# Optimization experiments

Hardware: AMD Instinct MI355X
Metric: run time of the kernel (lower is better)

The kernel has to match this reference:

```python
import jax, jax.numpy as jnp
import numpy as np

N = 50000       # total nodes
D = 20000       # disease nodes (first D rows)
M = 30000       # mirna nodes
E = 800000      # edges
DSIM = 512; MSIM = 512
HID = 128; OUT = 128; P = 3   # powers p = [0,1,2]
PAIRS = 100000


def _lin(k, o, i):
    s = 1.0 / np.sqrt(i)
    return jax.random.uniform(k, (o, i), jnp.float32, -s, s)


def setup_inputs() -> dict:
    key = jax.random.key(0)
    ks = jax.random.split(key, 24)
    inp = {}
    inp["d_sim"] = jax.random.normal(ks[0], (N, DSIM), jnp.float32)
    inp["m_sim"] = jax.random.normal(ks[1], (N, MSIM), jnp.float32)
    inp["edge_src"] = jax.random.randint(ks[2], (E,), 0, N, jnp.int32)
    inp["edge_dst"] = jax.random.randint(ks[3], (E,), 0, N, jnp.int32)
    inp["src"] = jax.random.randint(ks[4], (PAIRS,), 0, D, jnp.int32)
    inp["dst"] = D + jax.random.randint(ks[5], (PAIRS,), 0, M, jnp.int32)
    # input projections
    inp["d_fc_w"] = _lin(ks[6], HID, DSIM); inp["d_fc_b"] = jnp.zeros((HID,), jnp.float32)
    inp["m_fc_w"] = _lin(ks[7], HID, MSIM); inp["m_fc_b"] = jnp.zeros((HID,), jnp.float32)
    # MixHopConv per-power weights (no bias)
    inp["l0_w"] = jnp.stack([_lin(ks[8 + j], OUT, HID) for j in range(P)])         # [P, OUT, HID]
    inp["l1_w"] = jnp.stack([_lin(ks[11 + j], HID, OUT * P) for j in range(P)])    # [P, HID, OUT*P]
    inp["fc_w"] = _lin(ks[14], OUT, HID * P)
    inp["d_fc1_w"] = _lin(ks[15], OUT, OUT + DSIM); inp["d_fc1_b"] = jnp.zeros((OUT,), jnp.float32)
    inp["m_fc1_w"] = _lin(ks[16], OUT, OUT + MSIM); inp["m_fc1_b"] = jnp.zeros((OUT,), jnp.float32)
    # predictor MLP
    inp["p0_w"] = _lin(ks[17], OUT, 2 * OUT); inp["p0_b"] = jnp.zeros((OUT,), jnp.float32)
    inp["p1_w"] = _lin(ks[18], 1, OUT); inp["p1_b"] = jnp.zeros((1,), jnp.float32)
    return inp


def _mixhop(feats, Ws, edge_src, edge_dst, norm):
    """DGL MixHopConv with p=[0,1,2]: outputs [W_j (D^-1/2 A D^-1/2)^j X for j in p], concatenated."""
    outs = []
    for j in range(P):
        outs.append(feats @ Ws[j].T)
        if j < P - 1:  # propagate one more hop (last hop's propagation is unused)
            feats = feats * norm
            feats = jax.ops.segment_sum(feats[edge_src], edge_dst, num_segments=N)
            feats = feats * norm
    return jnp.concatenate(outs, axis=1)


def reference(d_sim, m_sim, edge_src, edge_dst, src, dst,
              d_fc_w, d_fc_b, m_fc_w, m_fc_b, l0_w, l1_w, fc_w,
              d_fc1_w, d_fc1_b, m_fc1_w, m_fc1_b, p0_w, p0_b, p1_w, p1_b):
    # symmetric normalization from in-degrees (clamped to >= 1)
    degs = jax.ops.segment_sum(jnp.ones((E,), jnp.float32), edge_dst, num_segments=N)
    norm = (jnp.maximum(degs, 1.0) ** -0.5)[:, None]  # [N, 1]
    # per-node-type input projection (dropout = identity in eval)
    z_d = d_sim[:D] @ d_fc_w.T + d_fc_b
    z_m = m_sim[D:] @ m_fc_w.T + m_fc_b
    feats = jnp.concatenate([z_d, z_m], axis=0)               # [N, HID]
    feats = _mixhop(feats, l0_w, edge_src, edge_dst, norm)    # [N, OUT*P]
    feats = _mixhop(feats, l1_w, edge_src, edge_dst, norm)    # [N, HID*P]
    feats = feats @ fc_w.T                                    # [N, OUT]
    h_d = jax.nn.elu(jnp.concatenate([feats[:D], d_sim[:D]], axis=1) @ d_fc1_w.T + d_fc1_b)
    h_m = jax.nn.elu(jnp.concatenate([feats[D:], m_sim[D:]], axis=1) @ m_fc1_w.T + m_fc1_b)
    h = jnp.concatenate([h_d, h_m], axis=0)                   # [N, OUT]
    hc = jnp.concatenate([h[src], h[dst]], axis=1)            # [PAIRS, 2*OUT]
    score = jax.nn.sigmoid(jax.nn.relu(hc @ p0_w.T + p0_b) @ p1_w.T + p1_b)
    return score
```

## Files before the change

kernel.cpp:

```cpp
#include <hip/hip_runtime.h>
#include <cstddef>
#include <cstdint>

#define N_NODES 50000
#define D_NODES 20000
#define M_NODES 30000
#define E_EDGES 800000
#define PAIRS_N 100000

typedef unsigned short u16;
typedef unsigned int u32;
typedef short bf16x8 __attribute__((ext_vector_type(8)));
typedef float f32x4 __attribute__((ext_vector_type(4)));

__device__ __forceinline__ float bf2f(u16 u) {
  u32 v = ((u32)u) << 16;
  return __builtin_bit_cast(float, v);
}
__device__ __forceinline__ u16 f2bf(float f) {
  u32 u = __builtin_bit_cast(u32, f);
  u32 r = (u + 0x7fffu + ((u >> 16) & 1u)) >> 16;
  return (u16)r;
}
__device__ __forceinline__ u32 pk2(float x, float y) {
  return (u32)f2bf(x) | ((u32)f2bf(y) << 16);
}

__global__ void simconv_kernel(const float* __restrict__ dsim, const float* __restrict__ msim,
                               u16* __restrict__ out) {
  int i = blockIdx.x * 256 + threadIdx.x;
  if (i >= N_NODES * 64) return;
  int row = i >> 6, c8 = (i & 63) << 3;
  const float* p = ((row < D_NODES) ? dsim : msim) + (size_t)row * 512 + c8;
  float4 f0 = ((const float4*)p)[0];
  float4 f1 = ((const float4*)p)[1];
  *(uint4*)(out + (size_t)i * 8) =
      make_uint4(pk2(f0.x, f0.y), pk2(f0.z, f0.w), pk2(f1.x, f1.y), pk2(f1.z, f1.w));
}

__global__ void wconv_kernel(const float* s0, const float* s1, const float* s2,
                             const float* s3, const float* s4,
                             u16* d0, u16* d1, u16* d2, u16* d3, u16* d4) {
  int i = blockIdx.x * 256 + threadIdx.x;
  const float* s; u16* d; int l;
  if      (i < 16384) { s = s0; d = d0; l = i; }
  else if (i < 32768) { s = s1; d = d1; l = i - 16384; }
  else if (i < 53248) { s = s2; d = d2; l = i - 32768; }
  else if (i < 73728) { s = s3; d = d3; l = i - 53248; }
  else if (i < 81920) { s = s4; d = d4; l = i - 73728; }
  else return;
  float4 v = *(const float4*)(s + (size_t)l * 4);
  ushort4 o;
  o.x = f2bf(v.x); o.y = f2bf(v.y); o.z = f2bf(v.z); o.w = f2bf(v.w);
  *(ushort4*)(d + (size_t)l * 4) = o;
}

__global__ void wcomb1_kernel(const float* __restrict__ l1w, const float* __restrict__ l0w,
                              float* __restrict__ Tmp) {
  int pj = blockIdx.x;
  int p = pj / 3, j = pj % 3;
  int o = blockIdx.y;
  int i = threadIdx.x;
  const float* wp = l1w + (size_t)p * 49152 + (size_t)o * 384 + 128 * j;
  const float* wj = l0w + (size_t)j * 16384 + i;
  float acc = 0.f;
#pragma unroll 4
  for (int t = 0; t < 128; ++t) acc += wp[t] * wj[(size_t)t * 128];
  Tmp[(size_t)pj * 16384 + (size_t)o * 128 + i] = acc;
}
__global__ void wcomb2_kernel(const float* __restrict__ fcw, const float* __restrict__ Tmp,
                              u16* __restrict__ G) {
  int k = blockIdx.x;
  int of = blockIdx.y;
  int i = threadIdx.x;
  float acc = 0.f;
  int plo = (k > 2) ? (k - 2) : 0;
  int phi = (k < 2) ? k : 2;
  for (int p = plo; p <= phi; ++p) {
    int j = k - p;
    const float* fp = fcw + (size_t)of * 384 + 128 * p;
    const float* tp = Tmp + (size_t)(p * 3 + j) * 16384 + i;
#pragma unroll 4
    for (int t = 0; t < 128; ++t) acc += fp[t] * tp[(size_t)t * 128];
  }
  G[(size_t)of * 640 + 128 * k + i] = f2bf(acc);
}

__global__ void zero_int_kernel(int* p, int n) {
  int i = blockIdx.x * 256 + threadIdx.x;
  if (i < n) p[i] = 0;
}
__global__ void deg_count_kernel(const int* __restrict__ dst, int* __restrict__ degs, int e) {
  int i = blockIdx.x * 256 + threadIdx.x;
  if (i < e) atomicAdd(&degs[dst[i]], 1);
}
__global__ void norm_reduce_kernel(const int* __restrict__ degs, float* __restrict__ norm,
                                   int n, int* __restrict__ bsums) {
  __shared__ int s[256];
  int t = threadIdx.x;
  int i = blockIdx.x * 256 + t;
  int d = (i < n) ? degs[i] : 0;
  if (i < n) norm[i] = rsqrtf(fmaxf((float)d, 1.0f));
  s[t] = d;
  __syncthreads();
  for (int st = 128; st > 0; st >>= 1) {
    if (t < st) s[t] += s[t + st];
    __syncthreads();
  }
  if (t == 0) bsums[blockIdx.x] = s[0];
}
__global__ void scan_small_kernel(int* b, int nb) {
  __shared__ int s[256];
  int t = threadIdx.x;
  int orig = (t < nb) ? b[t] : 0;
  s[t] = orig;
  __syncthreads();
  for (int st = 1; st < 256; st <<= 1) {
    int v = (t >= st) ? s[t - st] : 0;
    __syncthreads();
    s[t] += v;
    __syncthreads();
  }
  if (t < nb) b[t] = s[t] - orig;
}
__global__ void scan_final_kernel(const int* __restrict__ degs, const int* __restrict__ boff,
                                  int* __restrict__ out, int* __restrict__ cursor,
                                  int n, int total) {
  __shared__ int s[256];
  int t = threadIdx.x;
  int i = blockIdx.x * 256 + t;
  int orig = (i < n) ? degs[i] : 0;
  s[t] = orig;
  __syncthreads();
  for (int st = 1; st < 256; st <<= 1) {
    int v = (t >= st) ? s[t - st] : 0;
    __syncthreads();
    s[t] += v;
    __syncthreads();
  }
  if (i < n) {
    int v = boff[blockIdx.x] + s[t] - orig;
    out[i] = v;
    cursor[i] = v;
  }
  if (i == 0) out[n] = total;
}
__global__ void fill_csr_kernel(const int* __restrict__ esrc, const int* __restrict__ edst,
                                int* __restrict__ cursor, int* __restrict__ csr_src, int e) {
  int i = blockIdx.x * 256 + threadIdx.x;
  if (i < e) {
    int p = atomicAdd(&cursor[edst[i]], 1);
    csr_src[p] = esrc[i];
  }
}

__global__ void prop_kernel(const u16* __restrict__ in,
                            u16* __restrict__ outu, int ldu, int cOff,
                            u16* __restrict__ outs,
                            const int* __restrict__ off, const int* __restrict__ srcs,
                            const float* __restrict__ norm, int nnodes) {
  const int node = blockIdx.x * 4 + (threadIdx.x >> 6);
  if (node >= nnodes) return;
  const int lane = threadIdx.x & 63;
  const int e0 = off[node], e1 = off[node + 1];
  float a0 = 0.f, a1 = 0.f;
  const u16* basec = in + (lane << 1);
  for (int base = e0; base < e1; base += 64) {
    int nE = e1 - base; if (nE > 64) nE = 64;
    int myE = srcs[base + ((lane < nE) ? lane : (nE - 1))];
    int i = 0;
    for (; i + 8 <= nE; i += 8) {
      int s0 = __builtin_amdgcn_readlane(myE, i + 0);
      int s1 = __builtin_amdgcn_readlane(myE, i + 1);
      int s2 = __builtin_amdgcn_readlane(myE, i + 2);
      int s3 = __builtin_amdgcn_readlane(myE, i + 3);
      int s4 = __builtin_amdgcn_readlane(myE, i + 4);
      int s5 = __builtin_amdgcn_readlane(myE, i + 5);
      int s6 = __builtin_amdgcn_readlane(myE, i + 6);
      int s7 = __builtin_amdgcn_readlane(myE, i + 7);
      u32 v0 = *(const u32*)(basec + ((size_t)s0 << 7));
      u32 v1 = *(const u32*)(basec + ((size_t)s1 << 7));
      u32 v2 = *(const u32*)(basec + ((size_t)s2 << 7));
      u32 v3 = *(const u32*)(basec + ((size_t)s3 << 7));
      u32 v4 = *(const u32*)(basec + ((size_t)s4 << 7));
      u32 v5 = *(const u32*)(basec + ((size_t)s5 << 7));
      u32 v6 = *(const u32*)(basec + ((size_t)s6 << 7));
      u32 v7 = *(const u32*)(basec + ((size_t)s7 << 7));
      a0 += bf2f((u16)v0); a1 += bf2f((u16)(v0 >> 16));
      a0 += bf2f((u16)v1); a1 += bf2f((u16)(v1 >> 16));
      a0 += bf2f((u16)v2); a1 += bf2f((u16)(v2 >> 16));
      a0 += bf2f((u16)v3); a1 += bf2f((u16)(v3 >> 16));
      a0 += bf2f((u16)v4); a1 += bf2f((u16)(v4 >> 16));
      a0 += bf2f((u16)v5); a1 += bf2f((u16)(v5 >> 16));
      a0 += bf2f((u16)v6); a1 += bf2f((u16)(v6 >> 16));
      a0 += bf2f((u16)v7); a1 += bf2f((u16)(v7 >> 16));
    }
    for (; i < nE; ++i) {
      int s = __builtin_amdgcn_readlane(myE, i);
      u32 v = *(const u32*)(basec + ((size_t)s << 7));
      a0 += bf2f((u16)v); a1 += bf2f((u16)(v >> 16));
    }
  }
  float nd = norm[node];
  *(u32*)(outu + (size_t)node * ldu + cOff + (lane << 1)) = pk2(a0 * nd, a1 * nd);
  if (outs) {
    float nd2 = nd * nd;
    *(u32*)(outs + ((size_t)node << 7) + (lane << 1)) = pk2(a0 * nd2, a1 * nd2);
  }
}

__global__ __launch_bounds__(256) void mfma_gemm_kernel(
    const u16* __restrict__ A1, int lda1, int K1,
    const u16* __restrict__ A2, int lda2, int K2,
    const int* __restrict__ gsrc, const int* __restrict__ gdst,
    const u16* __restrict__ Wa, const u16* __restrict__ Wb,
    const float* __restrict__ biasa, const float* __restrict__ biasb,
    int splitB, int rowD, int boundA, int nrows,
    u16* __restrict__ Cu, int ldcu, int colOff,
    u16* __restrict__ Cs, const float* __restrict__ normp,
    const float* __restrict__ p1w, const float* __restrict__ p1b, float* __restrict__ outf,
    int act) {
  __shared__ u32 As[32 * 32];
  __shared__ u32 Ws[128 * 32];
  const int tid = threadIdx.x;
  const bool segb = (int)blockIdx.x >= splitB;
  const int brow = segb ? rowD + ((int)blockIdx.x - splitB) * 32 : (int)blockIdx.x * 32;
  const int bound = segb ? nrows : boundA;
  const u16* W = segb ? Wb : Wa;
  const float* bias = segb ? biasb : biasa;
  const int K = K1 + K2;
  const int lane = tid & 63;
  const int wv = tid >> 6;
  const int fr = lane & 15;
  const int fg = lane >> 4;

  f32x4 acc[2][2];
#pragma unroll
  for (int m = 0; m < 2; ++m)
#pragma unroll
    for (int n = 0; n < 2; ++n) acc[m][n] = (f32x4){0.f, 0.f, 0.f, 0.f};

  const int sr = tid >> 3, sk = tid & 7;
  const int swc = tid >> 1, sh = tid & 1;
  const int prow = (brow + sr < bound) ? (brow + sr) : (bound - 1);

  for (int kc = 0; kc < K; kc += 64) {
    uint4 qa;
    {
      bool seg1 = kc < K1;
      int kk = (seg1 ? kc : kc - K1) + sk * 8;
      const u16* Av = seg1 ? A1 : A2;
      int ld = seg1 ? lda1 : lda2;
      int row = gsrc ? (seg1 ? gsrc[prow] : gdst[prow]) : prow;
      qa = *(const uint4*)(Av + (size_t)row * ld + kk);
    }
    const u16* wp = W + (size_t)swc * K + kc + sh * 32;
    uint4 qw0 = *(const uint4*)(wp);
    uint4 qw1 = *(const uint4*)(wp + 8);
    uint4 qw2 = *(const uint4*)(wp + 16);
    uint4 qw3 = *(const uint4*)(wp + 24);

    __syncthreads();
    *(uint4*)&As[sr * 32 + (sk ^ (sr & 7)) * 4] = qa;
    *(uint4*)&Ws[swc * 32 + ((sh * 4 + 0) ^ (swc & 7)) * 4] = qw0;
    *(uint4*)&Ws[swc * 32 + ((sh * 4 + 1) ^ (swc & 7)) * 4] = qw1;
    *(uint4*)&Ws[swc * 32 + ((sh * 4 + 2) ^ (swc & 7)) * 4] = qw2;
    *(uint4*)&Ws[swc * 32 + ((sh * 4 + 3) ^ (swc & 7)) * 4] = qw3;
    __syncthreads();

#pragma unroll
    for (int kk2 = 0; kk2 < 2; ++kk2) {
      int gix = kk2 * 4 + fg;
      int r0 = fr, r1 = 16 + fr;
      bf16x8 aF0 = *(const bf16x8*)&As[r0 * 32 + (gix ^ (r0 & 7)) * 4];
      bf16x8 aF1 = *(const bf16x8*)&As[r1 * 32 + (gix ^ (r1 & 7)) * 4];
#pragma unroll
      for (int n = 0; n < 2; ++n) {
        int cr = wv * 32 + n * 16 + fr;
        bf16x8 bF = *(const bf16x8*)&Ws[cr * 32 + (gix ^ (cr & 7)) * 4];
        acc[0][n] = __builtin_amdgcn_mfma_f32_16x16x32_bf16(aF0, bF, acc[0][n], 0, 0, 0);
        acc[1][n] = __builtin_amdgcn_mfma_f32_16x16x32_bf16(aF1, bF, acc[1][n], 0, 0, 0);
      }
    }
  }

  if (act == 3) {
    float part[2][4];
#pragma unroll
    for (int m = 0; m < 2; ++m)
#pragma unroll
      for (int i = 0; i < 4; ++i) part[m][i] = 0.f;
#pragma unroll
    for (int n = 0; n < 2; ++n) {
      int ccol = wv * 32 + n * 16 + fr;
      float b = bias[ccol];
      float pw = p1w[ccol];
#pragma unroll
      for (int m = 0; m < 2; ++m)
#pragma unroll
        for (int i = 0; i < 4; ++i) {
          float v = acc[m][n][i] + b;
          v = fmaxf(v, 0.f);
          part[m][i] += v * pw;
        }
    }
#pragma unroll
    for (int mask = 1; mask <= 8; mask <<= 1)
#pragma unroll
      for (int m = 0; m < 2; ++m)
#pragma unroll
        for (int i = 0; i < 4; ++i) part[m][i] += __shfl_xor(part[m][i], mask);
    __syncthreads();
    float* sred = (float*)As;
    if (fr == 0) {
#pragma unroll
      for (int m = 0; m < 2; ++m)
#pragma unroll
        for (int i = 0; i < 4; ++i) sred[wv * 32 + m * 16 + fg * 4 + i] = part[m][i];
    }
    __syncthreads();
    if (tid < 32) {
      int row = brow + tid;
      if (row < bound) {
        float s = sred[tid] + sred[32 + tid] + sred[64 + tid] + sred[96 + tid] + p1b[0];
        outf[row] = 1.f / (1.f + expf(-s));
      }
    }
    return;
  }

#pragma unroll
  for (int m = 0; m < 2; ++m) {
#pragma unroll
    for (int n = 0; n < 2; ++n) {
      int ccol = wv * 32 + n * 16 + fr;
      float b = bias ? bias[ccol] : 0.f;
#pragma unroll
      for (int i = 0; i < 4; ++i) {
        int row = brow + m * 16 + fg * 4 + i;
        if (row < bound) {
          float v = acc[m][n][i] + b;
          if (act == 1) v = (v > 0.f) ? v : (expf(v) - 1.f);
          else if (act == 2) v = fmaxf(v, 0.f);
          Cu[(size_t)row * ldcu + colOff + ccol] = f2bf(v);
          if (Cs) Cs[((size_t)row << 7) + ccol] = f2bf(v * normp[row]);
        }
      }
    }
  }
}

extern "C" void kernel_launch(void* const* d_in, const int* in_sizes, int n_in,
                              void* d_out, int out_size, void* d_ws, size_t ws_size,
                              hipStream_t stream) {
  const float* d_sim   = (const float*)d_in[0];
  const float* m_sim   = (const float*)d_in[1];
  const int*   e_src   = (const int*)d_in[2];
  const int*   e_dst   = (const int*)d_in[3];
  const int*   p_src   = (const int*)d_in[4];
  const int*   p_dst   = (const int*)d_in[5];
  const float* d_fc_w  = (const float*)d_in[6];
  const float* d_fc_b  = (const float*)d_in[7];
  const float* m_fc_w  = (const float*)d_in[8];
  const float* m_fc_b  = (const float*)d_in[9];
  const float* l0_w    = (const float*)d_in[10];
  const float* l1_w    = (const float*)d_in[11];
  const float* fc_w    = (const float*)d_in[12];
  const float* d_fc1_w = (const float*)d_in[13];
  const float* d_fc1_b = (const float*)d_in[14];
  const float* m_fc1_w = (const float*)d_in[15];
  const float* m_fc1_b = (const float*)d_in[16];
  const float* p0_w    = (const float*)d_in[17];
  const float* p0_b    = (const float*)d_in[18];
  const float* p1_w    = (const float*)d_in[19];
  const float* p1_b    = (const float*)d_in[20];
  float* out = (float*)d_out;

  const int N = N_NODES, D = D_NODES, M = M_NODES, E = E_EDGES, NP = PAIRS_N;

  u16* ws16 = (u16*)d_ws;
  u16* HCAT = ws16;
  u16* SIMS = HCAT + (size_t)N * 640;
  u16* HSa  = SIMS + (size_t)N * 512;
  u16* HSb  = HSa + (size_t)N * 128;
  u16* FE   = HSb + (size_t)N * 128;
  u16* HB   = FE  + (size_t)N * 128;
  u16* wb_dfc  = HB + (size_t)N * 128;
  u16* wb_mfc  = wb_dfc  + 65536;
  u16* wb_dfc1 = wb_mfc  + 65536;
  u16* wb_mfc1 = wb_dfc1 + 81920;
  u16* wb_p0   = wb_mfc1 + 81920;
  u16* wb_G    = wb_p0   + 32768;
  u16* wend    = wb_G    + 81920;
  size_t off16 = (size_t)(wend - ws16);
  off16 = (off16 + 1) & ~(size_t)1;
  float* Tmp   = (float*)(ws16 + off16);
  float* normp = Tmp + 9 * 16384;
  int* degs    = (int*)(normp + N);
  int* csr_off = degs + N;
  int* cursor  = csr_off + N + 1;
  int* csr_src = cursor + N;
  int* bsums   = csr_src + E;

  const int nb = (N + 255) / 256;
  const int eb = (E + 255) / 256;

  wconv_kernel<<<320, 256, 0, stream>>>(d_fc_w, m_fc_w, d_fc1_w, m_fc1_w, p0_w,
                                        wb_dfc, wb_mfc, wb_dfc1, wb_mfc1, wb_p0);
  simconv_kernel<<<(N * 64 + 255) / 256, 256, 0, stream>>>(d_sim, m_sim, SIMS);
  wcomb1_kernel<<<dim3(9, 128), 128, 0, stream>>>(l1_w, l0_w, Tmp);
  wcomb2_kernel<<<dim3(5, 128), 128, 0, stream>>>(fc_w, Tmp, wb_G);

  zero_int_kernel<<<nb, 256, 0, stream>>>(degs, N);
  deg_count_kernel<<<eb, 256, 0, stream>>>(e_dst, degs, E);
  norm_reduce_kernel<<<nb, 256, 0, stream>>>(degs, normp, N, bsums);
  scan_small_kernel<<<1, 256, 0, stream>>>(bsums, nb);
  scan_final_kernel<<<nb, 256, 0, stream>>>(degs, bsums, csr_off, cursor, N, E);
  fill_csr_kernel<<<eb, 256, 0, stream>>>(e_src, e_dst, cursor, csr_src, E);

  const int GDseg = D / 32;
  const int GMseg = (M + 31) / 32;
  const int GSEG = GDseg + GMseg;
  const int GN = (N + 31) / 32;
  const int GP = (NP + 31) / 32;
  const int GPROP = (N + 3) / 4;

  mfma_gemm_kernel<<<GSEG, 256, 0, stream>>>(
      SIMS, 512, 512, nullptr, 0, 0, nullptr, nullptr,
      wb_dfc, wb_mfc, d_fc_b, m_fc_b, GDseg, D, D, N,
      HCAT, 640, 0, HSa, normp, nullptr, nullptr, nullptr, 0);

  prop_kernel<<<GPROP, 256, 0, stream>>>(HSa, HCAT, 640, 128, HSb, csr_off, csr_src, normp, N);
  prop_kernel<<<GPROP, 256, 0, stream>>>(HSb, HCAT, 640, 256, HSa, csr_off, csr_src, normp, N);
  prop_kernel<<<GPROP, 256, 0, stream>>>(HSa, HCAT, 640, 384, HSb, csr_off, csr_src, normp, N);
  prop_kernel<<<GPROP, 256, 0, stream>>>(HSb, HCAT, 640, 512, nullptr, csr_off, csr_src, normp, N);

  mfma_gemm_kernel<<<GN, 256, 0, stream>>>(
      HCAT, 640, 640, nullptr, 0, 0, nullptr, nullptr,
      wb_G, wb_G, nullptr, nullptr, GN, 0, N, N,
      FE, 128, 0, nullptr, normp, nullptr, nullptr, nullptr, 0);

  mfma_gemm_kernel<<<GSEG, 256, 0, stream>>>(
      FE, 128, 128, SIMS, 512, 512, nullptr, nullptr,
      wb_dfc1, wb_mfc1, d_fc1_b, m_fc1_b, GDseg, D, D, N,
      HB, 128, 0, nullptr, normp, nullptr, nullptr, nullptr, 1);

  mfma_gemm_kernel<<<GP, 256, 0, stream>>>(
      HB, 128, 128, HB, 128, 128, p_src, p_dst,
      wb_p0, wb_p0, p0_b, p0_b, GP, 0, NP, NP,
      nullptr, 128, 0, nullptr, normp, p1_w, p1_b, out, 3);

  (void)in_sizes; (void)n_in; (void)out_size; (void)ws_size;
}
```

Measured before the change: 398.9 us.

## Fuse sim projection with fc1 sim-part GEMM, drop bf16 sim copy

The fp32 similarity matrices are now read directly in a fused projection kernel that converts to bf16 in registers. The same kernel computes both the input projection and the sim half of the fc1 layer, using a combined 256-column weight, and stores the latter as fp32 partial sums. This removes the separate sim conversion pass and the second read of the sims in the fc1 GEMM. The GEMM kernels also gain register double-buffered prefetch of the next K-chunk. In exchange the code writes and re-reads an fp32 N×128 partial buffer and uses more LDS per block.

New measurement: 562.2 us. 1.41x slower.

```diff
diff --git a/kernel.cpp b/kernel.cpp
--- a/kernel.cpp
+++ b/kernel.cpp
@@ -26,33 +26,40 @@
   return (u32)f2bf(x) | ((u32)f2bf(y) << 16);
 }
 
-__global__ void simconv_kernel(const float* __restrict__ dsim, const float* __restrict__ msim,
-                               u16* __restrict__ out) {
+__global__ void wprep_kernel(const float* dfc, const float* mfc,
+                             const float* dfc1, const float* mfc1, const float* p0w,
+                             u16* dP, u16* mP, u16* dfc1f, u16* mfc1f, u16* p0b) {
   int i = blockIdx.x * 256 + threadIdx.x;
-  if (i >= N_NODES * 64) return;
-  int row = i >> 6, c8 = (i & 63) << 3;
-  const float* p = ((row < D_NODES) ? dsim : msim) + (size_t)row * 512 + c8;
-  float4 f0 = ((const float4*)p)[0];
-  float4 f1 = ((const float4*)p)[1];
-  *(uint4*)(out + (size_t)i * 8) =
-      make_uint4(pk2(f0.x, f0.y), pk2(f0.z, f0.w), pk2(f1.x, f1.y), pk2(f1.z, f1.w));
-}
-
-__global__ void wconv_kernel(const float* s0, const float* s1, const float* s2,
-                             const float* s3, const float* s4,
-                             u16* d0, u16* d1, u16* d2, u16* d3, u16* d4) {
-  int i = blockIdx.x * 256 + threadIdx.x;
-  const float* s; u16* d; int l;
-  if      (i < 16384) { s = s0; d = d0; l = i; }
-  else if (i < 32768) { s = s1; d = d1; l = i - 16384; }
-  else if (i < 53248) { s = s2; d = d2; l = i - 32768; }
-  else if (i < 73728) { s = s3; d = d3; l = i - 53248; }
-  else if (i < 81920) { s = s4; d = d4; l = i - 73728; }
-  else return;
-  float4 v = *(const float4*)(s + (size_t)l * 4);
-  ushort4 o;
-  o.x = f2bf(v.x); o.y = f2bf(v.y); o.z = f2bf(v.z); o.w = f2bf(v.w);
-  *(ushort4*)(d + (size_t)l * 4) = o;
+  const float* s; u16* d;
+  if (i < 16384) {
+    s = dfc + (size_t)i * 4; d = dP + (size_t)i * 4;
+  } else if (i < 32768) {
+    int l = i - 16384, o = l >> 7, kq = l & 127;
+    s = dfc1 + (size_t)o * 640 + 128 + kq * 4;
+    d = dP + (size_t)(128 + o) * 512 + kq * 4;
+  } else if (i < 49152) {
+    int l = i - 32768;
+    s = mfc + (size_t)l * 4; d = mP + (size_t)l * 4;
+  } else if (i < 65536) {
+    int l = i - 49152, o = l >> 7, kq = l & 127;
+    s = mfc1 + (size_t)o * 640 + 128 + kq * 4;
+    d = mP + (size_t)(128 + o) * 512 + kq * 4;
+  } else if (i < 69632) {
+    int l = i - 65536, o = l >> 5, kq = l & 31;
+    s = dfc1 + (size_t)o * 640 + kq * 4;
+    d = dfc1f + (size_t)o * 128 + kq * 4;
+  } else if (i < 73728) {
+    int l = i - 69632, o = l >> 5, kq = l & 31;
+    s = mfc1 + (size_t)o * 640 + kq * 4;
+    d = mfc1f + (size_t)o * 128 + kq * 4;
+  } else if (i < 81920) {
+    int l = i - 73728;
+    s = p0w + (size_t)l * 4; d = p0b + (size_t)l * 4;
+  } else return;
+  float4 v = *(const float4*)s;
+  ushort4 o4;
+  o4.x = f2bf(v.x); o4.y = f2bf(v.y); o4.z = f2bf(v.z); o4.w = f2bf(v.w);
+  *(ushort4*)d = o4;
 }
 
 __global__ void wcomb1_kernel(const float* __restrict__ l1w, const float* __restrict__ l0w,
@@ -209,30 +216,119 @@
   }
 }
 
-__global__ __launch_bounds__(256) void mfma_gemm_kernel(
+__global__ __launch_bounds__(256) void proj_fused_kernel(
+    const float* __restrict__ A1, const float* __restrict__ A2,
+    const u16* __restrict__ Wa, const u16* __restrict__ Wb,
+    const float* __restrict__ biasa, const float* __restrict__ biasb,
+    int splitB, u16* __restrict__ HCAT, u16* __restrict__ HSa,
+    float* __restrict__ SB, const float* __restrict__ normp) {
+  __shared__ u32 As[32 * 32];
+  __shared__ u32 Ws[256 * 32];
+  const int tid = threadIdx.x;
+  const int w = tid >> 6, lane = tid & 63;
+  const int fr = lane & 15, fg = lane >> 4;
+  const bool segb = (int)blockIdx.x >= splitB;
+  const int brow = segb ? D_NODES + ((int)blockIdx.x - splitB) * 32 : (int)blockIdx.x * 32;
+  const int bound = segb ? N_NODES : D_NODES;
+  const float* A = segb ? A2 : A1;
+  const u16* W = segb ? Wb : Wa;
+  const float* bias = segb ? biasb : biasa;
+  const int K = 512;
+  const int sr = tid >> 3, sk = tid & 7;
+  const int prow = (brow + sr < bound) ? (brow + sr) : (bound - 1);
+  const float* abase = A + (size_t)prow * 512 + sk * 8;
+  const u16* wrow = W + (size_t)tid * K;
+
+  f32x4 acc[2][4];
+#pragma unroll
+  for (int m = 0; m < 2; ++m)
+#pragma unroll
+    for (int n = 0; n < 4; ++n) acc[m][n] = (f32x4){0.f, 0.f, 0.f, 0.f};
+
+  float4 pf0, pf1;
+  uint4 pw[8];
+  pf0 = ((const float4*)abase)[0];
+  pf1 = ((const float4*)abase)[1];
+#pragma unroll
+  for (int j = 0; j < 8; ++j) pw[j] = *(const uint4*)(wrow + j * 8);
+
+  for (int kc = 0; kc < K; kc += 64) {
+    __syncthreads();
+    uint4 qa = make_uint4(pk2(pf0.x, pf0.y), pk2(pf0.z, pf0.w),
+                          pk2(pf1.x, pf1.y), pk2(pf1.z, pf1.w));
+    *(uint4*)&As[sr * 32 + (sk ^ (sr & 7)) * 4] = qa;
+#pragma unroll
+    for (int j = 0; j < 8; ++j) *(uint4*)&Ws[tid * 32 + (j ^ (tid & 7)) * 4] = pw[j];
+    __syncthreads();
+    if (kc + 64 < K) {
+      const float* ap = abase + kc + 64;
+      pf0 = ((const float4*)ap)[0];
+      pf1 = ((const float4*)ap)[1];
+      const u16* wp = wrow + kc + 64;
+#pragma unroll
+      for (int j = 0; j < 8; ++j) pw[j] = *(const uint4*)(wp + j * 8);
+    }
+#pragma unroll
+    for (int kk2 = 0; kk2 < 2; ++kk2) {
+      int gix = kk2 * 4 + fg;
+      int r0 = fr, r1 = 16 + fr;
+      bf16x8 aF0 = *(const bf16x8*)&As[r0 * 32 + (gix ^ (r0 & 7)) * 4];
+      bf16x8 aF1 = *(const bf16x8*)&As[r1 * 32 + (gix ^ (r1 & 7)) * 4];
+#pragma unroll
+      for (int n = 0; n < 4; ++n) {
+        int cr = w * 64 + n * 16 + fr;
+        bf16x8 bF = *(const bf16x8*)&Ws[cr * 32 + (gix ^ (cr & 7)) * 4];
+        acc[0][n] = __builtin_amdgcn_mfma_f32_16x16x32_bf16(aF0, bF, acc[0][n], 0, 0, 0);
+        acc[1][n] = __builtin_amdgcn_mfma_f32_16x16x32_bf16(aF1, bF, acc[1][n], 0, 0, 0);
+      }
+    }
+  }
+
+#pragma unroll
+  for (int m = 0; m < 2; ++m) {
+#pragma unroll
+    for (int n = 0; n < 4; ++n) {
+      int ccol = w * 64 + n * 16 + fr;
+#pragma unroll
+      for (int i = 0; i < 4; ++i) {
+        int row = brow + m * 16 + fg * 4 + i;
+        if (row < bound) {
+          if (ccol < 128) {
+            float v = acc[m][n][i] + bias[ccol];
+            HCAT[(size_t)row * 640 + ccol] = f2bf(v);
+            HSa[((size_t)row << 7) + ccol] = f2bf(v * normp[row]);
+          } else {
+            SB[((size_t)row << 7) + (ccol - 128)] = acc[m][n][i];
+          }
+        }
+      }
+    }
+  }
+}
+
+__global__ __launch_bounds__(256) void gemm128_kernel(
     const u16* __restrict__ A1, int lda1, int K1,
     const u16* __restrict__ A2, int lda2, int K2,
     const int* __restrict__ gsrc, const int* __restrict__ gdst,
     const u16* __restrict__ Wa, const u16* __restrict__ Wb,
     const float* __restrict__ biasa, const float* __restrict__ biasb,
     int splitB, int rowD, int boundA, int nrows,
-    u16* __restrict__ Cu, int ldcu, int colOff,
-    u16* __restrict__ Cs, const float* __restrict__ normp,
+    u16* __restrict__ Cu, int ldcu,
+    const float* __restrict__ SBadd,
     const float* __restrict__ p1w, const float* __restrict__ p1b, float* __restrict__ outf,
     int act) {
   __shared__ u32 As[32 * 32];
   __shared__ u32 Ws[128 * 32];
   const int tid = threadIdx.x;
+  const int lane = tid & 63;
+  const int wv = tid >> 6;
+  const int fr = lane & 15, fg = lane >> 4;
   const bool segb = (int)blockIdx.x >= splitB;
   const int brow = segb ? rowD + ((int)blockIdx.x - splitB) * 32 : (int)blockIdx.x * 32;
   const int bound = segb ? nrows : boundA;
   const u16* W = segb ? Wb : Wa;
   const float* bias = segb ? biasb : biasa;
   const int K = K1 + K2;
-  const int lane = tid & 63;
-  const int wv = tid >> 6;
-  const int fr = lane & 15;
-  const int fg = lane >> 4;
 
   f32x4 acc[2][2];
 #pragma unroll
@@ -243,31 +339,45 @@
   const int sr = tid >> 3, sk = tid & 7;
   const int swc = tid >> 1, sh = tid & 1;
   const int prow = (brow + sr < bound) ? (brow + sr) : (bound - 1);
+  const int rA = gsrc ? gsrc[prow] : prow;
+  const int rB = gsrc ? gdst[prow] : prow;
+  const u16* wrow = W + (size_t)swc * K + sh * 32;
+
+  uint4 pa, pw0, pw1, pw2, pw3;
+  {
+    bool seg1 = 0 < K1;
+    const u16* base = seg1 ? A1 : A2;
+    int ld = seg1 ? lda1 : lda2;
+    int row = seg1 ? rA : rB;
+    pa = *(const uint4*)(base + (size_t)row * ld + sk * 8);
+    pw0 = *(const uint4*)(wrow);
+    pw1 = *(const uint4*)(wrow + 8);
+    pw2 = *(const uint4*)(wrow + 16);
+    pw3 = *(const uint4*)(wrow + 24);
+  }
 
   for (int kc = 0; kc < K; kc += 64) {
-    uint4 qa;
-    {
-      bool seg1 = kc < K1;
-      int kk = (seg1 ? kc : kc - K1) + sk * 8;
-      const u16* Av = seg1 ? A1 : A2;
+    __syncthreads();
+    *(uint4*)&As[sr * 32 + (sk ^ (sr & 7)) * 4] = pa;
+    *(uint4*)&Ws[swc * 32 + ((sh * 4 + 0) ^ (swc & 7)) * 4] = pw0;
+    *(uint4*)&Ws[swc * 32 + ((sh * 4 + 1) ^ (swc & 7)) * 4] = pw1;
+    *(uint4*)&Ws[swc * 32 + ((sh * 4 + 2) ^ (swc & 7)) * 4] = pw2;
+    *(uint4*)&Ws[swc * 32 + ((sh * 4 + 3) ^ (swc & 7)) * 4] = pw3;
+    __syncthreads();
+    int kn = kc + 64;
+    if (kn < K) {
+      bool seg1 = kn < K1;
+      int kk = (seg1 ? kn : kn - K1) + sk * 8;
+      const u16* base = seg1 ? A1 : A2;
       int ld = seg1 ? lda1 : lda2;
-      int row = gsrc ? (seg1 ? gsrc[prow] : gdst[prow]) : prow;
-      qa = *(const uint4*)(Av + (size_t)row * ld + kk);
-    }
-    const u16* wp = W + (size_t)swc * K + kc + sh * 32;
-    uint4 qw0 = *(const uint4*)(wp);
-    uint4 qw1 = *(const uint4*)(wp + 8);
-    uint4 qw2 = *(const uint4*)(wp + 16);
-    uint4 qw3 = *(const uint4*)(wp + 24);
-
-    __syncthreads();
-    *(uint4*)&As[sr * 32 + (sk ^ (sr & 7)) * 4] = qa;
-    *(uint4*)&Ws[swc * 32 + ((sh * 4 + 0) ^ (swc & 7)) * 4] = qw0;
-    *(uint4*)&Ws[swc * 32 + ((sh * 4 + 1) ^ (swc & 7)) * 4] = qw1;
-    *(uint4*)&Ws[swc * 32 + ((sh * 4 + 2) ^ (swc & 7)) * 4] = qw2;
-    *(uint4*)&Ws[swc * 32 + ((sh * 4 + 3) ^ (swc & 7)) * 4] = qw3;
-    __syncthreads();
-
+      int row = seg1 ? rA : rB;
+      pa = *(const uint4*)(base + (size_t)row * ld + kk);
+      const u16* wp = wrow + kn;
+      pw0 = *(const uint4*)(wp);
+      pw1 = *(const uint4*)(wp + 8);
+      pw2 = *(const uint4*)(wp + 16);
+      pw3 = *(const uint4*)(wp + 24);
+    }
 #pragma unroll
     for (int kk2 = 0; kk2 < 2; ++kk2) {
       int gix = kk2 * 4 + fg;
@@ -299,8 +409,7 @@
       for (int m = 0; m < 2; ++m)
 #pragma unroll
         for (int i = 0; i < 4; ++i) {
-          float v = acc[m][n][i] + b;
-          v = fmaxf(v, 0.f);
+          float v = fmaxf(acc[m][n][i] + b, 0.f);
           part[m][i] += v * pw;
         }
     }
@@ -340,10 +449,9 @@
         int row = brow + m * 16 + fg * 4 + i;
         if (row < bound) {
           float v = acc[m][n][i] + b;
+          if (SBadd) v += SBadd[((size_t)row << 7) + ccol];
           if (act == 1) v = (v > 0.f) ? v : (expf(v) - 1.f);
-          else if (act == 2) v = fmaxf(v, 0.f);
-          Cu[(size_t)row * ldcu + colOff + ccol] = f2bf(v);
-          if (Cs) Cs[((size_t)row << 7) + ccol] = f2bf(v * normp[row]);
+          Cu[(size_t)row * ldcu + ccol] = f2bf(v);
         }
       }
     }
@@ -380,21 +488,21 @@
 
   u16* ws16 = (u16*)d_ws;
   u16* HCAT = ws16;
-  u16* SIMS = HCAT + (size_t)N * 640;
-  u16* HSa  = SIMS + (size_t)N * 512;
+  u16* HSa  = HCAT + (size_t)N * 640;
   u16* HSb  = HSa + (size_t)N * 128;
   u16* FE   = HSb + (size_t)N * 128;
   u16* HB   = FE  + (size_t)N * 128;
-  u16* wb_dfc  = HB + (size_t)N * 128;
-  u16* wb_mfc  = wb_dfc  + 65536;
-  u16* wb_dfc1 = wb_mfc  + 65536;
-  u16* wb_mfc1 = wb_dfc1 + 81920;
-  u16* wb_p0   = wb_mfc1 + 81920;
-  u16* wb_G    = wb_p0   + 32768;
-  u16* wend    = wb_G    + 81920;
+  u16* wb_dP    = HB + (size_t)N * 128;
+  u16* wb_mP    = wb_dP + 131072;
+  u16* wb_dfc1f = wb_mP + 131072;
+  u16* wb_mfc1f = wb_dfc1f + 16384;
+  u16* wb_p0    = wb_mfc1f + 16384;
+  u16* wb_G     = wb_p0 + 32768;
+  u16* wend     = wb_G + 81920;
   size_t off16 = (size_t)(wend - ws16);
   off16 = (off16 + 1) & ~(size_t)1;
-  float* Tmp   = (float*)(ws16 + off16);
+  float* SB    = (float*)(ws16 + off16);
+  float* Tmp   = SB + (size_t)N * 128;
   float* normp = Tmp + 9 * 16384;
   int* degs    = (int*)(normp + N);
   int* csr_off = degs + N;
@@ -405,9 +513,8 @@
   const int nb = (N + 255) / 256;
   const int eb = (E + 255) / 256;
 
-  wconv_kernel<<<320, 256, 0, stream>>>(d_fc_w, m_fc_w, d_fc1_w, m_fc1_w, p0_w,
-                                        wb_dfc, wb_mfc, wb_dfc1, wb_mfc1, wb_p0);
-  simconv_kernel<<<(N * 64 + 255) / 256, 256, 0, stream>>>(d_sim, m_sim, SIMS);
+  wprep_kernel<<<320, 256, 0, stream>>>(d_fc_w, m_fc_w, d_fc1_w, m_fc1_w, p0_w,
+                                        wb_dP, wb_mP, wb_dfc1f, wb_mfc1f, wb_p0);
   wcomb1_kernel<<<dim3(9, 128), 128, 0, stream>>>(l1_w, l0_w, Tmp);
   wcomb2_kernel<<<dim3(5, 128), 128, 0, stream>>>(fc_w, Tmp, wb_G);
 
@@ -418,37 +525,36 @@
   scan_final_kernel<<<nb, 256, 0, stream>>>(degs, bsums, csr_off, cursor, N, E);
   fill_csr_kernel<<<eb, 256, 0, stream>>>(e_src, e_dst, cursor, csr_src, E);
 
-  const int GDseg = D / 32;
+  const int GDseg = (D + 31) / 32;
   const int GMseg = (M + 31) / 32;
   const int GSEG = GDseg + GMseg;
   const int GN = (N + 31) / 32;
   const int GP = (NP + 31) / 32;
   const int GPROP = (N + 3) / 4;
 
-  mfma_gemm_kernel<<<GSEG, 256, 0, stream>>>(
-      SIMS, 512, 512, nullptr, 0, 0, nullptr, nullptr,
-      wb_dfc, wb_mfc, d_fc_b, m_fc_b, GDseg, D, D, N,
-      HCAT, 640, 0, HSa, normp, nullptr, nullptr, nullptr, 0);
+  proj_fused_kernel<<<GSEG, 256, 0, stream>>>(
+      d_sim, m_sim, wb_dP, wb_mP, d_fc_b, m_fc_b, GDseg,
+      HCAT, HSa, SB, normp);
 
   prop_kernel<<<GPROP, 256, 0, stream>>>(HSa, HCAT, 640, 128, HSb, csr_off, csr_src, normp, N);
   prop_kernel<<<GPROP, 256, 0, stream>>>(HSb, HCAT, 640, 256, HSa, csr_off, csr_src, normp, N);
   prop_kernel<<<GPROP, 256, 0, stream>>>(HSa, HCAT, 640, 384, HSb, csr_off, csr_src, normp, N);
   prop_kernel<<<GPROP, 256, 0, stream>>>(HSb, HCAT, 640, 512, nullptr, csr_off, csr_src, normp, N);
 
-  mfma_gemm_kernel<<<GN, 256, 0, stream>>>(
-      HCAT, 640, 640, nullptr, 0, 0, nullptr, nullptr,
+  gemm128_kernel<<<GN, 256, 0, stream>>>(
+      HCAT, 640, 640, HCAT, 640, 0, nullptr, nullptr,
       wb_G, wb_G, nullptr, nullptr, GN, 0, N, N,
-      FE, 128, 0, nullptr, normp, nullptr, nullptr, nullptr, 0);
-
-  mfma_gemm_kernel<<<GSEG, 256, 0, stream>>>(
-      FE, 128, 128, SIMS, 512, 512, nullptr, nullptr,
-      wb_dfc1, wb_mfc1, d_fc1_b, m_fc1_b, GDseg, D, D, N,
-      HB, 128, 0, nullptr, normp, nullptr, nullptr, nullptr, 1);
-
-  mfma_gemm_kernel<<<GP, 256, 0, stream>>>(
+      FE, 128, nullptr, nullptr, nullptr, nullptr, 0);
+
+  gemm128_kernel<<<GSEG, 256, 0, stream>>>(
+      FE, 128, 128, FE, 128, 0, nullptr, nullptr,
+      wb_dfc1f, wb_mfc1f, d_fc1_b, m_fc1_b, GDseg, D, D, N,
+      HB, 128, SB, nullptr, nullptr, nullptr, 1);
+
+  gemm128_kernel<<<GP, 256, 0, stream>>>(
       HB, 128, 128, HB, 128, 128, p_src, p_dst,
       wb_p0, wb_p0, p0_b, p0_b, GP, 0, NP, NP,
-      nullptr, 128, 0, nullptr, normp, p1_w, p1_b, out, 3);
+      nullptr, 128, nullptr, p1_w, p1_b, out, 3);
 
   (void)in_sizes; (void)n_in; (void)out_size; (void)ws_size;
 }
```
